# Kernel optimization log

Measured on AMD Instinct MI355X. Metric: run time of the kernel, lower is better.

The kernel has to match this reference:

```python
import jax, jax.numpy as jnp
import numpy as np

M, P, B, TLEN = 512, 256, 128, 1024

def setup_inputs() -> dict:
    key = jax.random.key(0)
    k1, k2, k3, k4, k5, k6 = jax.random.split(key, 6)
    d_t = jax.random.normal(k1, (1, B, P), dtype=jnp.float32)
    s_t = jax.random.normal(k2, (1, B, P), dtype=jnp.float32)
    H = jax.random.normal(k3, (B, TLEN, M), dtype=jnp.float32)
    # torch.nn.Linear weights: shape [out_features, in_features]
    W_d = jax.random.normal(k4, (M, 2 * P), dtype=jnp.float32) / np.sqrt(2 * P)
    U_d = jax.random.normal(k5, (M, M), dtype=jnp.float32) / np.sqrt(M)
    v_d = jax.random.normal(k6, (1, M), dtype=jnp.float32) / np.sqrt(M)
    return {"d_t": d_t, "s_t": s_t, "H": H, "T": TLEN, "W_d": W_d, "U_d": U_d, "v_d": v_d}

def reference(d_t, s_t, H, T, W_d, U_d, v_d):
    # query: cat([d_t, s_t], dim=2) -> [1, B, 2p]; permute(1,0,2) -> [B, 1, 2p]
    query = jnp.concatenate([d_t, s_t], axis=2).transpose(1, 0, 2)  # [B, 1, 2p]
    # W_d(query) broadcast over T instead of materializing the repeat (same math)
    wq = jnp.einsum('boc,mc->bom', query, W_d)          # [B, 1, m]
    uh = jnp.einsum('btm,nm->btn', H, U_d)              # [B, T, m]
    beta = jnp.tanh(wq + uh)                            # [B, T, m]
    score = jnp.einsum('btm,om->bto', beta, v_d)        # [B, T, 1]
    score = score.transpose(0, 2, 1)                    # [B, 1, T]
    return jax.nn.softmax(score, axis=2)
```

## Files before the change

kernel.cpp:

```cpp
#include <hip/hip_runtime.h>
#include <hip/hip_bf16.h>
#include <stdint.h>

#define NB   128
#define NT   1024
#define NM   512
#define NP   256

typedef __attribute__((ext_vector_type(8))) short bf16x8;
typedef __attribute__((ext_vector_type(4))) float f32x4;
typedef unsigned int u32;

__device__ __forceinline__ uint32_t bfpair(float a, float b) {
    uint32_t ua = __float_as_uint(a) + 0x8000u;
    uint32_t ub = __float_as_uint(b) + 0x8000u;
    return __builtin_amdgcn_perm(ub, ua, 0x07060302u);
}

__device__ __forceinline__ float fast_tanh(float x) {
    float e = __expf(2.0f * x);
    return 1.0f - 2.0f * __builtin_amdgcn_rcpf(e + 1.0f);
}

typedef const __attribute__((address_space(1))) u32* gas_t;
typedef __attribute__((address_space(3))) u32* las_t;
__device__ __forceinline__ void dma16(const void* g, void* l) {
    __builtin_amdgcn_global_load_lds((gas_t)g, (las_t)l, 16, 0, 0);
}

__global__ void prep_kernel(const float* __restrict__ U, unsigned short* __restrict__ Ub,
                            const float* __restrict__ d_t, const float* __restrict__ s_t,
                            const float* __restrict__ W, float* __restrict__ wq,
                            float* __restrict__ out) {
    const int bx = blockIdx.x;
    if (bx < 256) {
        int idx = bx * 256 + threadIdx.x;
        float4 u = reinterpret_cast<const float4*>(U)[idx];
        reinterpret_cast<uint2*>(Ub)[idx] = make_uint2(bfpair(u.x, u.y), bfpair(u.z, u.w));
    } else if (bx < 384) {
        int g = (bx - 256) * 512 + threadIdx.x * 2;
        int b = g >> 9;
        const float* dt = d_t + (size_t)b * NP;
        const float* st = s_t + (size_t)b * NP;
        #pragma unroll
        for (int e = 0; e < 2; ++e) {
            int n = (g + e) & 511;
            const float* Wn = W + (size_t)n * 512;
            float s = 0.f;
            #pragma unroll 4
            for (int c = 0; c < NP; c += 4) {
                float4 w0 = *reinterpret_cast<const float4*>(Wn + c);
                float4 q0 = *reinterpret_cast<const float4*>(dt + c);
                s += w0.x * q0.x + w0.y * q0.y + w0.z * q0.z + w0.w * q0.w;
                float4 w1 = *reinterpret_cast<const float4*>(Wn + NP + c);
                float4 q1 = *reinterpret_cast<const float4*>(st + c);
                s += w1.x * q1.x + w1.y * q1.y + w1.z * q1.z + w1.w * q1.w;
            }
            wq[g + e] = s;
        }
    } else {
        int idx = (bx - 384) * 256 + threadIdx.x;
        reinterpret_cast<float4*>(out)[idx] = make_float4(0.f, 0.f, 0.f, 0.f);
    }
}

__global__ __launch_bounds__(512, 4)
void score_kernel(const float* __restrict__ H, const unsigned short* __restrict__ Ub,
                  const float* __restrict__ wq, const float* __restrict__ v_d,
                  float* __restrict__ out) {
    __shared__ unsigned short As[2][128 * 32];
    __shared__ unsigned short Bs[3][256 * 32];
    __shared__ float s_score[128];

    const int tid  = threadIdx.x;
    const int id   = blockIdx.x;
    const int tile = (id >> 4) * 8 + (id & 7);
    const int nh   = (id >> 3) & 1;
    const int tt   = tile & 7;
    const int b    = tile >> 3;

    const int lane = tid & 63;
    const int w    = tid >> 6;
    const int lr   = lane & 15;
    const int lq   = lane >> 4;
    const int tw   = w >> 2;
    const int nw   = w & 3;

    if (tid < 128) s_score[tid] = 0.f;

    const int rA = tid >> 2, uA = tid & 3;
    const float* gA = H + ((size_t)(b * NT + tt * 128 + rA)) * NM + uA * 8;
    const u32 woff = (u32)(rA * 64 + ((uA ^ ((rA >> 1) & 3)) << 4));

    const unsigned short* gB0, * gB1;
    u32 lB0, lB1;
    {
        int rB0 = w * 32 + (lane >> 2);
        int rB1 = rB0 + 16;
        gB0 = Ub + ((size_t)(nh * 256 + rB0)) * NM + (((lane & 3) ^ ((rB0 >> 1) & 3)) * 8);
        gB1 = Ub + ((size_t)(nh * 256 + rB1)) * NM + (((lane & 3) ^ ((rB1 >> 1) & 3)) * 8);
        lB0 = (u32)((w * 32) * 64 + lane * 16);
        lB1 = lB0 + 16 * 64;
    }

    const u32 aro = (u32)((tw * 64 + lr) * 64 + ((lq ^ ((lr >> 1) & 3)) << 4));
    const u32 bro = (u32)((nw * 64 + lr) * 64 + ((lq ^ ((lr >> 1) & 3)) << 4));

    f32x4 acc[4][4];
    #pragma unroll
    for (int i = 0; i < 4; ++i)
        #pragma unroll
        for (int j = 0; j < 4; ++j)
            acc[i][j] = (f32x4){0.f, 0.f, 0.f, 0.f};

    float4 av0 = *reinterpret_cast<const float4*>(gA);
    float4 av1 = *reinterpret_cast<const float4*>(gA + 4);
    gA += 32;
    dma16(gB0, (char*)Bs[0] + lB0);
    dma16(gB1, (char*)Bs[0] + lB1);
    gB0 += 32; gB1 += 32;
    dma16(gB0, (char*)Bs[1] + lB0);
    dma16(gB1, (char*)Bs[1] + lB1);
    gB0 += 32; gB1 += 32;
    {
        uint4 wv4;
        wv4.x = bfpair(av0.x, av0.y); wv4.y = bfpair(av0.z, av0.w);
        wv4.z = bfpair(av1.x, av1.y); wv4.w = bfpair(av1.z, av1.w);
        *reinterpret_cast<uint4*>((char*)As[0] + woff) = wv4;
    }
    asm volatile("s_waitcnt vmcnt(2)" ::: "memory");
    asm volatile("s_waitcnt lgkmcnt(0)" ::: "memory");
    __builtin_amdgcn_s_barrier();
    __builtin_amdgcn_sched_barrier(0);

    u32 offA = 0;
    u32 rb0 = 0, rb1 = 16384, rb2 = 32768;

    #pragma unroll 1
    for (int kk = 0; kk < 16; ++kk) {
        const char* ab = (const char*)As + offA + aro;
        bf16x8 a0 = *reinterpret_cast<const bf16x8*>(ab);
        bf16x8 a1 = *reinterpret_cast<const bf16x8*>(ab + 1024);
        bf16x8 a2 = *reinterpret_cast<const bf16x8*>(ab + 2048);
        bf16x8 a3 = *reinterpret_cast<const bf16x8*>(ab + 3072);

        float4 nv0, nv1;
        if (kk < 15) {
            nv0 = *reinterpret_cast<const float4*>(gA);
            nv1 = *reinterpret_cast<const float4*>(gA + 4);
            gA += 32;
        }
        if (kk < 14) {
            char* bwr = (char*)Bs + rb2;
            dma16(gB0, bwr + lB0);
            dma16(gB1, bwr + lB1);
            gB0 += 32; gB1 += 32;
        }

        const char* bb = (const char*)Bs + rb0 + bro;
        #pragma unroll
        for (int j = 0; j < 4; ++j) {
            bf16x8 bj = *reinterpret_cast<const bf16x8*>(bb + j * 1024);
            acc[0][j] = __builtin_amdgcn_mfma_f32_16x16x32_bf16(a0, bj, acc[0][j], 0, 0, 0);
            acc[1][j] = __builtin_amdgcn_mfma_f32_16x16x32_bf16(a1, bj, acc[1][j], 0, 0, 0);
            acc[2][j] = __builtin_amdgcn_mfma_f32_16x16x32_bf16(a2, bj, acc[2][j], 0, 0, 0);
            acc[3][j] = __builtin_amdgcn_mfma_f32_16x16x32_bf16(a3, bj, acc[3][j], 0, 0, 0);
        }

        if (kk < 15) {
            char* an = (char*)As + (offA ^ 8192) + woff;
            uint4 wv4;
            wv4.x = bfpair(nv0.x, nv0.y); wv4.y = bfpair(nv0.z, nv0.w);
            wv4.z = bfpair(nv1.x, nv1.y); wv4.w = bfpair(nv1.z, nv1.w);
            *reinterpret_cast<uint4*>(an) = wv4;
            asm volatile("s_waitcnt vmcnt(2)" ::: "memory");
            asm volatile("s_waitcnt lgkmcnt(0)" ::: "memory");
            __builtin_amdgcn_s_barrier();
            __builtin_amdgcn_sched_barrier(0);
        }
        offA ^= 8192;
        u32 t = rb0; rb0 = rb1; rb1 = rb2; rb2 = t;
    }

    const float* wqb = wq + (size_t)b * NM;
    float vv[4], wv[4];
    #pragma unroll
    for (int j = 0; j < 4; ++j) {
        int n = nh * 256 + nw * 64 + j * 16 + lr;
        vv[j] = v_d[n];
        wv[j] = wqb[n];
    }
    #pragma unroll
    for (int i = 0; i < 4; ++i) {
        #pragma unroll
        for (int r = 0; r < 4; ++r) {
            float s = 0.f;
            #pragma unroll
            for (int j = 0; j < 4; ++j)
                s += vv[j] * fast_tanh(wv[j] + acc[i][j][r]);
            #pragma unroll
            for (int off = 1; off < 16; off <<= 1)
                s += __shfl_xor(s, off, 64);
            if (lr == 0) atomicAdd(&s_score[tw * 64 + i * 16 + lq * 4 + r], s);
        }
    }
    __syncthreads();
    if (tid < 128) atomicAdd(&out[(size_t)b * NT + tt * 128 + tid], s_score[tid]);
}

__global__ void softmax_kernel(float* __restrict__ out) {
    const int b   = blockIdx.x;
    const int tid = threadIdx.x;
    float* p = out + (size_t)b * NT;
    float4 v = reinterpret_cast<float4*>(p)[tid];
    float m = fmaxf(fmaxf(v.x, v.y), fmaxf(v.z, v.w));
    #pragma unroll
    for (int off = 32; off >= 1; off >>= 1)
        m = fmaxf(m, __shfl_xor(m, off, 64));
    __shared__ float red[8];
    const int wv = tid >> 6;
    if ((tid & 63) == 0) red[wv] = m;
    __syncthreads();
    m = fmaxf(fmaxf(red[0], red[1]), fmaxf(red[2], red[3]));
    float e0 = __expf(v.x - m), e1 = __expf(v.y - m);
    float e2 = __expf(v.z - m), e3 = __expf(v.w - m);
    float s = e0 + e1 + e2 + e3;
    #pragma unroll
    for (int off = 32; off >= 1; off >>= 1)
        s += __shfl_xor(s, off, 64);
    if ((tid & 63) == 0) red[4 + wv] = s;
    __syncthreads();
    s = red[4] + red[5] + red[6] + red[7];
    float inv = 1.f / s;
    float4 o;
    o.x = e0 * inv; o.y = e1 * inv; o.z = e2 * inv; o.w = e3 * inv;
    reinterpret_cast<float4*>(p)[tid] = o;
}

extern "C" void kernel_launch(void* const* d_in, const int* in_sizes, int n_in,
                              void* d_out, int out_size, void* d_ws, size_t ws_size,
                              hipStream_t stream) {
    const float* d_t = (const float*)d_in[0];
    const float* s_t = (const float*)d_in[1];
    const float* H   = (const float*)d_in[2];
    const float* W_d = (const float*)d_in[4];
    const float* U_d = (const float*)d_in[5];
    const float* v_d = (const float*)d_in[6];
    float* out = (float*)d_out;

    unsigned short* Ub = (unsigned short*)d_ws;
    float* wq = (float*)((char*)d_ws + 512 * 1024);

    prep_kernel<<<512, 256, 0, stream>>>(U_d, Ub, d_t, s_t, W_d, wq, out);
    score_kernel<<<2048, 512, 0, stream>>>(H, Ub, wq, v_d, out);
    softmax_kernel<<<NB, 256, 0, stream>>>(out);
}
```

Baseline: 464.0 us.

## Widen K-tile to 64, unroll pipelined main loop, use hardware bf16 convert

Reworks the score GEMM main loop to use 64-wide K steps (8 stages instead of 16). Each stage is split into two MFMA halves with setprio around the MFMA bursts, and the loop is fully unrolled. LDS grows to 128KB with a new XOR swizzle, so occupancy drops to 2 blocks per CU. The software bf16 rounding is replaced with v_cvt_pk_bf16_f32. The epilogue now writes per-lane partial sums to a padded LDS buffer and reduces with vector loads instead of shuffles plus LDS atomics. The aim is fewer barriers per unit of work and better overlap of loads with MFMA, at the cost of occupancy and more barriers inside each stage.

```diff
diff --git a/kernel.cpp b/kernel.cpp
--- a/kernel.cpp
+++ b/kernel.cpp
@@ -15,6 +15,12 @@
     uint32_t ua = __float_as_uint(a) + 0x8000u;
     uint32_t ub = __float_as_uint(b) + 0x8000u;
     return __builtin_amdgcn_perm(ub, ua, 0x07060302u);
+}
+
+__device__ __forceinline__ u32 cvtpk(float lo, float hi) {
+    u32 d;
+    asm("v_cvt_pk_bf16_f32 %0, %1, %2" : "=v"(d) : "v"(lo), "v"(hi));
+    return d;
 }
 
 __device__ __forceinline__ float fast_tanh(float x) {
@@ -64,13 +70,13 @@
     }
 }
 
-__global__ __launch_bounds__(512, 4)
+__global__ __launch_bounds__(512, 2)
 void score_kernel(const float* __restrict__ H, const unsigned short* __restrict__ Ub,
                   const float* __restrict__ wq, const float* __restrict__ v_d,
                   float* __restrict__ out) {
-    __shared__ unsigned short As[2][128 * 32];
-    __shared__ unsigned short Bs[3][256 * 32];
-    __shared__ float s_score[128];
+    __shared__ __align__(16) unsigned char smem[131072];
+    char* AsB = (char*)smem;
+    char* BsB = (char*)smem + 32768;
 
     const int tid  = threadIdx.x;
     const int id   = blockIdx.x;
@@ -86,25 +92,23 @@
     const int tw   = w >> 2;
     const int nw   = w & 3;
 
-    if (tid < 128) s_score[tid] = 0.f;
-
-    const int rA = tid >> 2, uA = tid & 3;
-    const float* gA = H + ((size_t)(b * NT + tt * 128 + rA)) * NM + uA * 8;
-    const u32 woff = (u32)(rA * 64 + ((uA ^ ((rA >> 1) & 3)) << 4));
-
-    const unsigned short* gB0, * gB1;
-    u32 lB0, lB1;
-    {
-        int rB0 = w * 32 + (lane >> 2);
-        int rB1 = rB0 + 16;
-        gB0 = Ub + ((size_t)(nh * 256 + rB0)) * NM + (((lane & 3) ^ ((rB0 >> 1) & 3)) * 8);
-        gB1 = Ub + ((size_t)(nh * 256 + rB1)) * NM + (((lane & 3) ^ ((rB1 >> 1) & 3)) * 8);
-        lB0 = (u32)((w * 32) * 64 + lane * 16);
-        lB1 = lB0 + 16 * 64;
-    }
-
-    const u32 aro = (u32)((tw * 64 + lr) * 64 + ((lq ^ ((lr >> 1) & 3)) << 4));
-    const u32 bro = (u32)((nw * 64 + lr) * 64 + ((lq ^ ((lr >> 1) & 3)) << 4));
+    const int rA = tid >> 2, seg = tid & 3;
+    const float* gA = H + ((size_t)(b * NT + tt * 128 + rA)) * NM + seg * 16;
+    const u32 woff0 = (u32)(rA * 128 + (((2 * seg) ^ (rA & 7)) << 4));
+    const u32 woff1 = woff0 ^ 16;
+
+    const unsigned short* gBq[4];
+    u32 lBq[4];
+    const u32 sOffB = (u32)(((lane & 7) ^ (lane >> 3)) * 8);
+    #pragma unroll
+    for (int q = 0; q < 4; ++q) {
+        int r = (w * 4 + q) * 8 + (lane >> 3);
+        gBq[q] = Ub + (size_t)(nh * 256 + r) * NM + sOffB;
+        lBq[q] = (u32)((w * 4 + q) * 1024 + lane * 16);
+    }
+
+    const u32 aoff = (u32)((tw * 64 + lr) * 128 + ((lq ^ (lr & 7)) << 4));
+    const u32 boff = (u32)((nw * 64 + lr) * 128 + ((lq ^ (lr & 7)) << 4));
 
     f32x4 acc[4][4];
     #pragma unroll
@@ -113,75 +117,93 @@
         for (int j = 0; j < 4; ++j)
             acc[i][j] = (f32x4){0.f, 0.f, 0.f, 0.f};
 
-    float4 av0 = *reinterpret_cast<const float4*>(gA);
-    float4 av1 = *reinterpret_cast<const float4*>(gA + 4);
-    gA += 32;
-    dma16(gB0, (char*)Bs[0] + lB0);
-    dma16(gB1, (char*)Bs[0] + lB1);
-    gB0 += 32; gB1 += 32;
-    dma16(gB0, (char*)Bs[1] + lB0);
-    dma16(gB1, (char*)Bs[1] + lB1);
-    gB0 += 32; gB1 += 32;
+    float4 av0[4], av1[4];
+    #pragma unroll
+    for (int q = 0; q < 4; ++q) av0[q] = *reinterpret_cast<const float4*>(gA + q * 4);
+    #pragma unroll
+    for (int q = 0; q < 4; ++q) dma16(gBq[q], BsB + lBq[q]);
+    #pragma unroll
+    for (int q = 0; q < 4; ++q) dma16(gBq[q] + 64, BsB + 32768 + lBq[q]);
     {
-        uint4 wv4;
-        wv4.x = bfpair(av0.x, av0.y); wv4.y = bfpair(av0.z, av0.w);
-        wv4.z = bfpair(av1.x, av1.y); wv4.w = bfpair(av1.z, av1.w);
-        *reinterpret_cast<uint4*>((char*)As[0] + woff) = wv4;
-    }
-    asm volatile("s_waitcnt vmcnt(2)" ::: "memory");
+        uint4 w0, w1;
+        w0.x = cvtpk(av0[0].x, av0[0].y); w0.y = cvtpk(av0[0].z, av0[0].w);
+        w0.z = cvtpk(av0[1].x, av0[1].y); w0.w = cvtpk(av0[1].z, av0[1].w);
+        w1.x = cvtpk(av0[2].x, av0[2].y); w1.y = cvtpk(av0[2].z, av0[2].w);
+        w1.z = cvtpk(av0[3].x, av0[3].y); w1.w = cvtpk(av0[3].z, av0[3].w);
+        *reinterpret_cast<uint4*>(AsB + woff0) = w0;
+        *reinterpret_cast<uint4*>(AsB + woff1) = w1;
+    }
+    #pragma unroll
+    for (int q = 0; q < 4; ++q) av1[q] = *reinterpret_cast<const float4*>(gA + 64 + q * 4);
+    asm volatile("s_waitcnt vmcnt(8)" ::: "memory");
     asm volatile("s_waitcnt lgkmcnt(0)" ::: "memory");
     __builtin_amdgcn_s_barrier();
     __builtin_amdgcn_sched_barrier(0);
 
-    u32 offA = 0;
-    u32 rb0 = 0, rb1 = 16384, rb2 = 32768;
-
-    #pragma unroll 1
-    for (int kk = 0; kk < 16; ++kk) {
-        const char* ab = (const char*)As + offA + aro;
-        bf16x8 a0 = *reinterpret_cast<const bf16x8*>(ab);
-        bf16x8 a1 = *reinterpret_cast<const bf16x8*>(ab + 1024);
-        bf16x8 a2 = *reinterpret_cast<const bf16x8*>(ab + 2048);
-        bf16x8 a3 = *reinterpret_cast<const bf16x8*>(ab + 3072);
-
-        float4 nv0, nv1;
-        if (kk < 15) {
-            nv0 = *reinterpret_cast<const float4*>(gA);
-            nv1 = *reinterpret_cast<const float4*>(gA + 4);
-            gA += 32;
+    #pragma unroll
+    for (int s = 0; s < 8; ++s) {
+        const char* ab = AsB + (s & 1) * 16384;
+        const char* bb = BsB + (s % 3) * 32768;
+
+        #pragma unroll
+        for (int kh = 0; kh < 2; ++kh) {
+            const u32 X = kh ? 64u : 0u;
+            bf16x8 a0 = *reinterpret_cast<const bf16x8*>(ab + (aoff ^ X));
+            bf16x8 a1 = *reinterpret_cast<const bf16x8*>(ab + (aoff ^ X) + 2048);
+            bf16x8 a2 = *reinterpret_cast<const bf16x8*>(ab + (aoff ^ X) + 4096);
+            bf16x8 a3 = *reinterpret_cast<const bf16x8*>(ab + (aoff ^ X) + 6144);
+            bf16x8 b0 = *reinterpret_cast<const bf16x8*>(bb + (boff ^ X));
+            bf16x8 b1 = *reinterpret_cast<const bf16x8*>(bb + (boff ^ X) + 2048);
+            bf16x8 b2 = *reinterpret_cast<const bf16x8*>(bb + (boff ^ X) + 4096);
+            bf16x8 b3 = *reinterpret_cast<const bf16x8*>(bb + (boff ^ X) + 6144);
+
+            if (kh == 0) {
+                if (s < 6) {
+                    char* bwr = BsB + ((s + 2) % 3) * 32768;
+                    #pragma unroll
+                    for (int q = 0; q < 4; ++q)
+                        dma16(gBq[q] + (size_t)(s + 2) * 64, bwr + lBq[q]);
+                }
+                if (s < 7) {
+                    float4 (&S)[4] = ((s + 1) & 1) ? av1 : av0;
+                    char* an = AsB + ((s + 1) & 1) * 16384;
+                    uint4 w0, w1;
+                    w0.x = cvtpk(S[0].x, S[0].y); w0.y = cvtpk(S[0].z, S[0].w);
+                    w0.z = cvtpk(S[1].x, S[1].y); w0.w = cvtpk(S[1].z, S[1].w);
+                    w1.x = cvtpk(S[2].x, S[2].y); w1.y = cvtpk(S[2].z, S[2].w);
+                    w1.z = cvtpk(S[3].x, S[3].y); w1.w = cvtpk(S[3].z, S[3].w);
+                    *reinterpret_cast<uint4*>(an + woff0) = w0;
+                    *reinterpret_cast<uint4*>(an + woff1) = w1;
+                }
+                if (s < 6) {
+                    float4 (&D)[4] = (s & 1) ? av1 : av0;
+                    #pragma unroll
+                    for (int q = 0; q < 4; ++q)
+                        D[q] = *reinterpret_cast<const float4*>(gA + (size_t)(s + 2) * 64 + q * 4);
+                }
+            }
+
+            __builtin_amdgcn_s_barrier();
+            asm volatile("s_waitcnt lgkmcnt(0)" ::: "memory");
+            __builtin_amdgcn_sched_barrier(0);
+            __builtin_amdgcn_s_setprio(1);
+            #pragma unroll
+            for (int j = 0; j < 4; ++j) {
+                bf16x8 bj = (j == 0) ? b0 : (j == 1) ? b1 : (j == 2) ? b2 : b3;
+                acc[0][j] = __builtin_amdgcn_mfma_f32_16x16x32_bf16(a0, bj, acc[0][j], 0, 0, 0);
+                acc[1][j] = __builtin_amdgcn_mfma_f32_16x16x32_bf16(a1, bj, acc[1][j], 0, 0, 0);
+                acc[2][j] = __builtin_amdgcn_mfma_f32_16x16x32_bf16(a2, bj, acc[2][j], 0, 0, 0);
+                acc[3][j] = __builtin_amdgcn_mfma_f32_16x16x32_bf16(a3, bj, acc[3][j], 0, 0, 0);
+            }
+            __builtin_amdgcn_s_setprio(0);
+            if (kh == 1 && s < 6) {
+                asm volatile("s_waitcnt vmcnt(4)" ::: "memory");
+            }
+            __builtin_amdgcn_s_barrier();
         }
-        if (kk < 14) {
-            char* bwr = (char*)Bs + rb2;
-            dma16(gB0, bwr + lB0);
-            dma16(gB1, bwr + lB1);
-            gB0 += 32; gB1 += 32;
-        }
-
-        const char* bb = (const char*)Bs + rb0 + bro;
-        #pragma unroll
-        for (int j = 0; j < 4; ++j) {
-            bf16x8 bj = *reinterpret_cast<const bf16x8*>(bb + j * 1024);
-            acc[0][j] = __builtin_amdgcn_mfma_f32_16x16x32_bf16(a0, bj, acc[0][j], 0, 0, 0);
-            acc[1][j] = __builtin_amdgcn_mfma_f32_16x16x32_bf16(a1, bj, acc[1][j], 0, 0, 0);
-            acc[2][j] = __builtin_amdgcn_mfma_f32_16x16x32_bf16(a2, bj, acc[2][j], 0, 0, 0);
-            acc[3][j] = __builtin_amdgcn_mfma_f32_16x16x32_bf16(a3, bj, acc[3][j], 0, 0, 0);
-        }
-
-        if (kk < 15) {
-            char* an = (char*)As + (offA ^ 8192) + woff;
-            uint4 wv4;
-            wv4.x = bfpair(nv0.x, nv0.y); wv4.y = bfpair(nv0.z, nv0.w);
-            wv4.z = bfpair(nv1.x, nv1.y); wv4.w = bfpair(nv1.z, nv1.w);
-            *reinterpret_cast<uint4*>(an) = wv4;
-            asm volatile("s_waitcnt vmcnt(2)" ::: "memory");
-            asm volatile("s_waitcnt lgkmcnt(0)" ::: "memory");
-            __builtin_amdgcn_s_barrier();
-            __builtin_amdgcn_sched_barrier(0);
-        }
-        offA ^= 8192;
-        u32 t = rb0; rb0 = rb1; rb1 = rb2; rb2 = t;
-    }
-
+    }
+
+    float* red = (float*)BsB;
     const float* wqb = wq + (size_t)b * NM;
     float vv[4], wv[4];
     #pragma unroll
@@ -198,14 +220,23 @@
             #pragma unroll
             for (int j = 0; j < 4; ++j)
                 s += vv[j] * fast_tanh(wv[j] + acc[i][j][r]);
-            #pragma unroll
-            for (int off = 1; off < 16; off <<= 1)
-                s += __shfl_xor(s, off, 64);
-            if (lr == 0) atomicAdd(&s_score[tw * 64 + i * 16 + lq * 4 + r], s);
+            red[(tw * 64 + i * 16 + lq * 4 + r) * 68 + nw * 16 + lr] = s;
         }
     }
     __syncthreads();
-    if (tid < 128) atomicAdd(&out[(size_t)b * NT + tt * 128 + tid], s_score[tid]);
+    {
+        const int t = tid >> 2, q = tid & 3;
+        const float* rp = red + (size_t)t * 68 + q * 16;
+        float4 x0 = *reinterpret_cast<const float4*>(rp);
+        float4 x1 = *reinterpret_cast<const float4*>(rp + 4);
+        float4 x2 = *reinterpret_cast<const float4*>(rp + 8);
+        float4 x3 = *reinterpret_cast<const float4*>(rp + 12);
+        float s = (x0.x + x0.y + x0.z + x0.w) + (x1.x + x1.y + x1.z + x1.w)
+                + (x2.x + x2.y + x2.z + x2.w) + (x3.x + x3.y + x3.z + x3.w);
+        s += __shfl_xor(s, 1, 64);
+        s += __shfl_xor(s, 2, 64);
+        if (q == 0) atomicAdd(&out[(size_t)b * NT + tt * 128 + t], s);
+    }
 }
 
 __global__ void softmax_kernel(float* __restrict__ out) {
```

After: 498.8 us. 1.08x slower.
